# Performance work log

Hardware: AMD Instinct MI355X
Metric: run time of the kernel (lower is better)

Reference implementation:

```python
import jax, jax.numpy as jnp
import numpy as np

BETA = 0.25


def setup_inputs() -> dict:
    key = jax.random.key(0)
    k1, k2 = jax.random.split(key)
    B, T, D, K = 16, 4096, 256, 4096
    z_e = jax.random.normal(k1, (B, T, D), dtype=jnp.float32)
    # emulate uniform(-1/K, 1/K) init but any values work for correctness
    codebook = jax.random.uniform(k2, (K, D), dtype=jnp.float32,
                                  minval=-1.0 / K, maxval=1.0 / K)
    return {"z_e": z_e, "codebook": codebook}


def reference(z_e, codebook):
    D = codebook.shape[1]
    z_flat = z_e.reshape(-1, D)                                  # [N, D]
    # squared L2 distances: ||z||^2 + ||e||^2 - 2 z.e
    z_norm = jnp.sum(z_flat ** 2, axis=1, keepdims=True)          # [N, 1]
    e_norm = jnp.sum(codebook ** 2, axis=1)                       # [K]
    dist = z_norm + e_norm - 2.0 * jnp.matmul(z_flat, codebook.T) # [N, K]
    idx_flat = jnp.argmin(dist, axis=1)                           # [N]
    idx = idx_flat.reshape(z_e.shape[:-1])                        # [B, T]
    z_q = codebook[idx]                                           # [B, T, D]
    # commitment loss: beta * mse(stop_grad(z_q), z_e)
    loss = BETA * jnp.mean((jax.lax.stop_gradient(z_q) - z_e) ** 2)
    # straight-through estimator
    z_q_st = z_e + jax.lax.stop_gradient(z_q - z_e)
    return z_q_st, idx, loss
```

## Files before the change

kernel.cpp:

```cpp
#include <hip/hip_runtime.h>
#include <cfloat>

#define NROWS 65536
#define DIM   256
#define KCB   4096

#define EPS_WIN  1.8e-4f
#define CAND_CAP 16

typedef __attribute__((ext_vector_type(8))) short short8;
typedef __attribute__((ext_vector_type(4))) float f32x4;

__device__ inline unsigned short f2bf(float x) {
  unsigned int u = __float_as_uint(x);
  return (unsigned short)((u + 0x7fffu + ((u >> 16) & 1u)) >> 16);
}

__global__ void prep_norms_kernel(const float* __restrict__ z, const float* __restrict__ cb,
                                  unsigned short* __restrict__ zh, unsigned short* __restrict__ eh,
                                  float* __restrict__ znorm, float* __restrict__ enorm) {
  const int r    = blockIdx.x * 4 + (threadIdx.x >> 6);
  const int lane = threadIdx.x & 63;
  const float* src; unsigned short* dst; float* nrm; int row;
  if (r < NROWS) { src = z;  dst = zh; nrm = znorm; row = r; }
  else           { src = cb; dst = eh; nrm = enorm; row = r - NROWS; }
  const float4 v = ((const float4*)(src + (size_t)row * DIM))[lane];
  union { unsigned short us[4]; uint2 u2; } o;
  o.us[0] = f2bf(v.x); o.us[1] = f2bf(v.y); o.us[2] = f2bf(v.z); o.us[3] = f2bf(v.w);
  *(uint2*)(dst + (size_t)row * DIM + lane * 4) = o.u2;
  float s = v.x * v.x + v.y * v.y + v.z * v.z + v.w * v.w;
  #pragma unroll
  for (int off = 32; off > 0; off >>= 1) s += __shfl_down(s, off);
  if (lane == 0) nrm[row] = s;
}

__launch_bounds__(256, 2)
__global__ void screen_kernel(const unsigned short* __restrict__ zh,
                              const unsigned short* __restrict__ eh,
                              const float* __restrict__ znorm,
                              const float* __restrict__ enorm,
                              unsigned int* __restrict__ counts,
                              unsigned short* __restrict__ cands) {
  __shared__ __align__(16) unsigned short a_s[128 * 256];
  __shared__ __align__(16) unsigned short b_s[128 * 32];
  __shared__ float zn_s[128];
  __shared__ float tilemin_s[2][128];
  __shared__ unsigned int cnt_s[128];
  __shared__ unsigned short cand_s[128 * CAND_CAP];

  const int tid = threadIdx.x;
  const int wv  = tid >> 6;
  const int ln  = tid & 63;
  const int l15 = ln & 15;
  const int lg  = ln >> 4;
  const int wr  = wv >> 1;
  const int wc  = wv & 1;
  const int rbase = blockIdx.x * 128;

  if (tid < 128) { zn_s[tid] = znorm[rbase + tid]; cnt_s[tid] = 0u; }

  #pragma unroll 1
  for (int i = 0; i < 16; ++i) {
    const int gid = i * 256 + tid;
    const int row = gid >> 5, slot = gid & 31;
    const int sw  = slot ^ (row & 7);
    *(uint4*)(&a_s[row * 256 + sw * 8]) =
        *(const uint4*)(&zh[(size_t)(rbase + row) * 256 + slot * 8]);
  }
  __syncthreads();

  float znv[16];
  #pragma unroll
  for (int fr = 0; fr < 4; ++fr)
    #pragma unroll
    for (int q = 0; q < 4; ++q)
      znv[fr * 4 + q] = zn_s[wr * 64 + fr * 16 + lg * 4 + q];

  float rm[16];
  #pragma unroll
  for (int s = 0; s < 16; ++s) rm[s] = FLT_MAX;

  #pragma unroll 1
  for (int kt = 0; kt < KCB / 128; ++kt) {
    const int kcb0 = kt * 128;
    f32x4 acc[4][4];
    #pragma unroll
    for (int fr = 0; fr < 4; ++fr)
      #pragma unroll
      for (int fc = 0; fc < 4; ++fc)
        acc[fr][fc] = (f32x4){0.f, 0.f, 0.f, 0.f};

    #pragma unroll 1
    for (int dc = 0; dc < 8; ++dc) {
      __syncthreads();
      #pragma unroll
      for (int i = 0; i < 2; ++i) {
        const int c  = i * 64 + wv * 16 + l15;
        const int sw = lg ^ ((c >> 1) & 3);
        *(uint4*)(&b_s[c * 32 + sw * 8]) =
            *(const uint4*)(&eh[(size_t)(kcb0 + c) * 256 + dc * 32 + lg * 8]);
      }
      __syncthreads();

      short8 af[4];
      #pragma unroll
      for (int fr = 0; fr < 4; ++fr) {
        const int r = wr * 64 + fr * 16 + l15;
        const int sl = (dc * 4 + lg) ^ (r & 7);
        af[fr] = *(const short8*)(&a_s[r * 256 + sl * 8]);
      }
      short8 bf[4];
      #pragma unroll
      for (int fc = 0; fc < 4; ++fc) {
        const int c = wc * 64 + fc * 16 + l15;
        const int sw = lg ^ ((c >> 1) & 3);
        bf[fc] = *(const short8*)(&b_s[c * 32 + sw * 8]);
      }
      #pragma unroll
      for (int fr = 0; fr < 4; ++fr)
        #pragma unroll
        for (int fc = 0; fc < 4; ++fc)
          acc[fr][fc] = __builtin_amdgcn_mfma_f32_16x16x32_bf16(
              af[fr], bf[fc], acc[fr][fc], 0, 0, 0);
    }

    float en_[4];
    #pragma unroll
    for (int fc = 0; fc < 4; ++fc) en_[fc] = enorm[kcb0 + wc * 64 + fc * 16 + l15];

    float tm[16];
    #pragma unroll
    for (int s = 0; s < 16; ++s) tm[s] = FLT_MAX;

    #pragma unroll
    for (int fr = 0; fr < 4; ++fr)
      #pragma unroll
      for (int fc = 0; fc < 4; ++fc)
        #pragma unroll
        for (int q = 0; q < 4; ++q) {
          const float d_ = fmaf(-2.0f, acc[fr][fc][q], znv[fr * 4 + q] + en_[fc]);
          tm[fr * 4 + q] = fminf(tm[fr * 4 + q], d_);
        }

    float hv[16];
    #pragma unroll
    for (int s = 0; s < 16; ++s) {
      float v = tm[s];
      v = fminf(v, __shfl_xor(v, 1));
      v = fminf(v, __shfl_xor(v, 2));
      v = fminf(v, __shfl_xor(v, 4));
      v = fminf(v, __shfl_xor(v, 8));
      hv[s] = v;
      if (l15 == 0) {
        const int fr = s >> 2, q = s & 3;
        tilemin_s[wc][wr * 64 + fr * 16 + lg * 4 + q] = v;
      }
    }
    __syncthreads();

    float th[16];
    float guard = 1.0f;
    #pragma unroll
    for (int s = 0; s < 16; ++s) {
      const int fr = s >> 2, q = s & 3;
      const float other = tilemin_s[wc ^ 1][wr * 64 + fr * 16 + lg * 4 + q];
      const float m = fminf(rm[s], fminf(hv[s], other));
      rm[s] = m;
      th[s] = m + EPS_WIN;
      guard = fminf(guard, tm[s] - th[s]);
    }

    if (__any(guard <= 0.0f)) {
      #pragma unroll
      for (int fr = 0; fr < 4; ++fr)
        #pragma unroll
        for (int fc = 0; fc < 4; ++fc)
          #pragma unroll
          for (int q = 0; q < 4; ++q) {
            const float d_ = fmaf(-2.0f, acc[fr][fc][q], znv[fr * 4 + q] + en_[fc]);
            if (d_ <= th[fr * 4 + q]) {
              const int rl = wr * 64 + fr * 16 + lg * 4 + q;
              const unsigned int pos = atomicAdd(&cnt_s[rl], 1u);
              if (pos < CAND_CAP)
                cand_s[rl * CAND_CAP + pos] =
                    (unsigned short)(kcb0 + wc * 64 + fc * 16 + l15);
            }
          }
    }
  }

  __syncthreads();
  if (tid < 128) counts[rbase + tid] = cnt_s[tid];
  for (int i = tid; i < 128 * CAND_CAP; i += 256)
    cands[(size_t)rbase * CAND_CAP + i] = cand_s[i];
}

__global__ void rescore_kernel(const float* __restrict__ z, const float* __restrict__ cb,
                               const float* __restrict__ znorm, const float* __restrict__ enorm,
                               const unsigned int* __restrict__ counts,
                               const unsigned short* __restrict__ cands,
                               int* __restrict__ idx) {
  const int gw  = (blockIdx.x * 256 + threadIdx.x) >> 6;
  const int ln  = threadIdx.x & 63;
  const int row = gw * 4 + (ln >> 4);
  const int ci  = ln & 15;
  const unsigned int cnt = counts[row];

  float bv = FLT_MAX; int bk = 0x7fffffff;
  if (cnt <= CAND_CAP) {
    const int active = ci < (int)cnt;
    const int k = active ? (int)cands[(size_t)row * CAND_CAP + ci] : 0;
    const float4* zr = (const float4*)(z  + (size_t)row * DIM);
    const float4* er = (const float4*)(cb + (size_t)k   * DIM);
    float ax = 0.f, ay = 0.f, az = 0.f, aw = 0.f;
    #pragma unroll 4
    for (int d = 0; d < DIM / 4; ++d) {
      const float4 zv = zr[d], ev = er[d];
      ax = fmaf(zv.x, ev.x, ax); ay = fmaf(zv.y, ev.y, ay);
      az = fmaf(zv.z, ev.z, az); aw = fmaf(zv.w, ev.w, aw);
    }
    const float acc = (ax + ay) + (az + aw);
    const float dist = fmaf(-2.0f, acc, znorm[row] + enorm[k]);
    if (active) { bv = dist; bk = k; }
  }
  #pragma unroll
  for (int off = 1; off < 16; off <<= 1) {
    const float ov = __shfl_xor(bv, off);
    const int   ok = __shfl_xor(bk, off);
    if (ov < bv || (ov == bv && ok < bk)) { bv = ov; bk = ok; }
  }
  if (ci == 0 && cnt <= CAND_CAP) idx[row] = bk;
}

__global__ void fallback_kernel(const float* __restrict__ z, const float* __restrict__ cb,
                                const float* __restrict__ znorm, const float* __restrict__ enorm,
                                const unsigned int* __restrict__ counts,
                                int* __restrict__ idx) {
  __shared__ float bd_s[256];
  __shared__ int   bk_s[256];
  const int tid = threadIdx.x;
  for (int row = blockIdx.x; row < NROWS; row += gridDim.x) {
    if (counts[row] <= CAND_CAP) continue;
    const float zn = znorm[row];
    const float* zr = z + (size_t)row * DIM;
    float bv = FLT_MAX; int bk = 0x7fffffff;
    for (int k = tid; k < KCB; k += 256) {
      const float* er = cb + (size_t)k * DIM;
      float acc = 0.0f;
      #pragma unroll 8
      for (int d = 0; d < DIM; ++d) acc = fmaf(zr[d], er[d], acc);
      const float dist = fmaf(-2.0f, acc, zn + enorm[k]);
      if (dist < bv || (dist == bv && k < bk)) { bv = dist; bk = k; }
    }
    bd_s[tid] = bv; bk_s[tid] = bk;
    __syncthreads();
    for (int s = 128; s > 0; s >>= 1) {
      if (tid < s) {
        const float ov = bd_s[tid + s]; const int ok = bk_s[tid + s];
        if (ov < bd_s[tid] || (ov == bd_s[tid] && ok < bk_s[tid])) {
          bd_s[tid] = ov; bk_s[tid] = ok;
        }
      }
      __syncthreads();
    }
    if (tid == 0) idx[row] = bk_s[0];
    __syncthreads();
  }
}

__global__ void norms_kernel(const float* __restrict__ x, float* __restrict__ out) {
  const int row  = blockIdx.x * 4 + (threadIdx.x >> 6);
  const int lane = threadIdx.x & 63;
  const float4 v = ((const float4*)(x + (size_t)row * DIM))[lane];
  float s = v.x * v.x + v.y * v.y + v.z * v.z + v.w * v.w;
  #pragma unroll
  for (int off = 32; off > 0; off >>= 1) s += __shfl_down(s, off);
  if (lane == 0) out[row] = s;
}

#define BM 128
#define BK 128
#define BD 32
#define LSTR 36
__launch_bounds__(256, 2)
__global__ void argmin_kernel(const float* __restrict__ z,
                              const float* __restrict__ cb,
                              const float* __restrict__ znorm,
                              const float* __restrict__ enorm,
                              int* __restrict__ idx_out) {
  __shared__ float z_s[BM * LSTR];
  __shared__ float e_s[BK * LSTR];
  __shared__ float zn_s[BM];
  const int tid = threadIdx.x;
  const int tx = tid & 15;
  const int ty = tid >> 4;
  const int rbase = blockIdx.x * BM;
  if (tid < BM) zn_s[tid] = znorm[rbase + tid];
  float bestv[8]; int besti[8];
  #pragma unroll
  for (int i = 0; i < 8; ++i) { bestv[i] = FLT_MAX; besti[i] = 0; }
  for (int kc = 0; kc < KCB; kc += BK) {
    float acc[8][8];
    #pragma unroll
    for (int i = 0; i < 8; ++i)
      #pragma unroll
      for (int j = 0; j < 8; ++j) acc[i][j] = 0.0f;
    for (int dc = 0; dc < DIM; dc += BD) {
      __syncthreads();
      #pragma unroll
      for (int p = 0; p < 4; ++p) {
        const int el = p * 256 + tid;
        const int r  = el >> 3;
        const int c4 = (el & 7) * 4;
        *(float4*)(&z_s[r * LSTR + c4]) =
            *(const float4*)(z + (size_t)(rbase + r) * DIM + dc + c4);
        *(float4*)(&e_s[r * LSTR + c4]) =
            *(const float4*)(cb + (size_t)(kc + r) * DIM + dc + c4);
      }
      __syncthreads();
      #pragma unroll 1
      for (int dd = 0; dd < BD; dd += 4) {
        float4 b[8];
        #pragma unroll
        for (int j = 0; j < 8; ++j)
          b[j] = *(const float4*)(&e_s[(tx + 16 * j) * LSTR + dd]);
        #pragma unroll
        for (int i = 0; i < 8; ++i) {
          const float4 a = *(const float4*)(&z_s[(ty + 16 * i) * LSTR + dd]);
          #pragma unroll
          for (int j = 0; j < 8; ++j)
            acc[i][j] += a.x * b[j].x + a.y * b[j].y + a.z * b[j].z + a.w * b[j].w;
        }
      }
    }
    float en[8];
    #pragma unroll
    for (int j = 0; j < 8; ++j) en[j] = enorm[kc + tx + 16 * j];
    #pragma unroll
    for (int i = 0; i < 8; ++i) {
      const float zn = zn_s[ty + 16 * i];
      #pragma unroll
      for (int j = 0; j < 8; ++j) {
        const float t1 = zn + en[j];
        const float dist = t1 - 2.0f * acc[i][j];
        const int k = kc + tx + 16 * j;
        if (dist < bestv[i]) { bestv[i] = dist; besti[i] = k; }
      }
    }
  }
  #pragma unroll
  for (int i = 0; i < 8; ++i) {
    float lv = bestv[i]; int li = besti[i];
    #pragma unroll
    for (int off = 1; off < 16; off <<= 1) {
      const float ov = __shfl_xor(lv, off);
      const int   oi = __shfl_xor(li, off);
      if (ov < lv || (ov == lv && oi < li)) { lv = ov; li = oi; }
    }
    if (tx == 0) idx_out[rbase + ty + 16 * i] = li;
  }
}

__global__ void gather_kernel(const float* __restrict__ z,
                              const float* __restrict__ cb,
                              const int* __restrict__ idx,
                              float* __restrict__ out_zq,
                              float* __restrict__ out_idx,
                              float* __restrict__ partials) {
  const int row  = blockIdx.x * 4 + (threadIdx.x >> 6);
  const int lane = threadIdx.x & 63;
  const int k = idx[row];
  const float4 zv = ((const float4*)(z  + (size_t)row * DIM))[lane];
  const float4 ev = ((const float4*)(cb + (size_t)k   * DIM))[lane];
  float4 d, st;
  d.x = ev.x - zv.x; d.y = ev.y - zv.y; d.z = ev.z - zv.z; d.w = ev.w - zv.w;
  st.x = zv.x + d.x; st.y = zv.y + d.y; st.z = zv.z + d.z; st.w = zv.w + d.w;
  ((float4*)(out_zq + (size_t)row * DIM))[lane] = st;
  if (lane == 0) out_idx[row] = (float)k;
  float s = d.x * d.x + d.y * d.y + d.z * d.z + d.w * d.w;
  #pragma unroll
  for (int off = 32; off > 0; off >>= 1) s += __shfl_down(s, off);
  __shared__ float ps[4];
  if (lane == 0) ps[threadIdx.x >> 6] = s;
  __syncthreads();
  if (threadIdx.x == 0)
    partials[blockIdx.x] = (ps[0] + ps[1]) + (ps[2] + ps[3]);
}

__global__ void loss_kernel(const float* __restrict__ partials,
                            float* __restrict__ out_loss) {
  float s = 0.0f;
  for (int i = threadIdx.x; i < NROWS / 4; i += 256) s += partials[i];
  #pragma unroll
  for (int off = 32; off > 0; off >>= 1) s += __shfl_down(s, off);
  __shared__ float ps[4];
  if ((threadIdx.x & 63) == 0) ps[threadIdx.x >> 6] = s;
  __syncthreads();
  if (threadIdx.x == 0)
    *out_loss = 0.25f * (((ps[0] + ps[1]) + (ps[2] + ps[3])) *
                         (1.0f / (float)((size_t)NROWS * DIM)));
}

extern "C" void kernel_launch(void* const* d_in, const int* in_sizes, int n_in,
                              void* d_out, int out_size, void* d_ws, size_t ws_size,
                              hipStream_t stream) {
  const float* z  = (const float*)d_in[0];
  const float* cb = (const float*)d_in[1];

  float* out_zq   = (float*)d_out;
  float* out_idx  = out_zq + (size_t)NROWS * DIM;
  float* out_loss = out_idx + NROWS;

  char* w = (char*)d_ws;
  unsigned short* zh    = (unsigned short*)(w);
  unsigned short* eh    = (unsigned short*)(w + 33554432);
  float* enorm          = (float*)(w + 35651584);
  float* znorm          = (float*)(w + 35667968);
  int*   idx            = (int*)(w + 35930112);
  unsigned int* counts  = (unsigned int*)(w + 36192256);
  unsigned short* cands = (unsigned short*)(w + 36454400);
  float* partials       = (float*)(w + 38551552);
  const size_t NEED = 38617088;

  if (ws_size >= NEED) {
    hipLaunchKernelGGL(prep_norms_kernel, dim3((NROWS + KCB) / 4), dim3(256), 0, stream,
                       z, cb, zh, eh, znorm, enorm);
    hipLaunchKernelGGL(screen_kernel, dim3(NROWS / 128), dim3(256), 0, stream,
                       zh, eh, znorm, enorm, counts, cands);
    hipLaunchKernelGGL(rescore_kernel, dim3(NROWS / 16), dim3(256), 0, stream,
                       z, cb, znorm, enorm, counts, cands, idx);
    hipLaunchKernelGGL(fallback_kernel, dim3(256), dim3(256), 0, stream,
                       z, cb, znorm, enorm, counts, idx);
    hipLaunchKernelGGL(gather_kernel, dim3(NROWS / 4), dim3(256), 0, stream,
                       z, cb, idx, out_zq, out_idx, partials);
    hipLaunchKernelGGL(loss_kernel, dim3(1), dim3(256), 0, stream, partials, out_loss);
  } else {
    float* ws        = (float*)d_ws;
    float* enorm_l   = ws;
    float* znorm_l   = ws + KCB;
    int*   idx_l     = (int*)(ws + KCB + NROWS);
    float* partials_l= ws + KCB + 2 * NROWS;
    hipLaunchKernelGGL(norms_kernel, dim3(KCB / 4), dim3(256), 0, stream, cb, enorm_l);
    hipLaunchKernelGGL(norms_kernel, dim3(NROWS / 4), dim3(256), 0, stream, z, znorm_l);
    hipLaunchKernelGGL(argmin_kernel, dim3(NROWS / BM), dim3(256), 0, stream,
                       z, cb, znorm_l, enorm_l, idx_l);
    hipLaunchKernelGGL(gather_kernel, dim3(NROWS / 4), dim3(256), 0, stream,
                       z, cb, idx_l, out_zq, out_idx, partials_l);
    hipLaunchKernelGGL(loss_kernel, dim3(1), dim3(256), 0, stream, partials_l, out_loss);
  }
}
```

Measured before the change: 520.5 us.

## Register-prefetch next codebook chunk and re-layout A tile into per-chunk panels

Codebook bf16 chunks are now loaded into registers one iteration ahead, so the global load for the next dc chunk overlaps with the MFMA work on the current one instead of stalling between the two barriers. The A tile in shared memory is reorganized into 8 panels of 128x32 with a swizzle matching the B tile, and the thread-to-element mapping for B loads is changed to contiguous 16-byte segments. This adds register pressure and one extra redundant prefetch at the final iteration, which wraps around to chunk 0.

```diff
diff --git a/kernel.cpp b/kernel.cpp
--- a/kernel.cpp
+++ b/kernel.cpp
@@ -41,7 +41,7 @@
                               const float* __restrict__ enorm,
                               unsigned int* __restrict__ counts,
                               unsigned short* __restrict__ cands) {
-  __shared__ __align__(16) unsigned short a_s[128 * 256];
+  __shared__ __align__(16) unsigned short a_s[8][128][32];
   __shared__ __align__(16) unsigned short b_s[128 * 32];
   __shared__ float zn_s[128];
   __shared__ float tilemin_s[2][128];
@@ -63,11 +63,24 @@
   for (int i = 0; i < 16; ++i) {
     const int gid = i * 256 + tid;
     const int row = gid >> 5, slot = gid & 31;
-    const int sw  = slot ^ (row & 7);
-    *(uint4*)(&a_s[row * 256 + sw * 8]) =
+    const int ch = slot >> 2, s4 = slot & 3;
+    const int sw = s4 ^ ((row >> 1) & 3);
+    *(uint4*)(&a_s[ch][row][sw * 8]) =
         *(const uint4*)(&zh[(size_t)(rbase + row) * 256 + slot * 8]);
   }
-  __syncthreads();
+
+  int pc[2], ps[2];
+  #pragma unroll
+  for (int t = 0; t < 2; ++t) {
+    const int o = wv * 2048 + t * 1024 + ln * 16;
+    pc[t] = o >> 6;
+    ps[t] = (o >> 4) & 3;
+  }
+
+  uint4 pre[2];
+  #pragma unroll
+  for (int t = 0; t < 2; ++t)
+    pre[t] = *(const uint4*)(&eh[(size_t)pc[t] * 256 + ps[t] * 8]);
 
   float znv[16];
   #pragma unroll
@@ -79,6 +92,8 @@
   float rm[16];
   #pragma unroll
   for (int s = 0; s < 16; ++s) rm[s] = FLT_MAX;
+
+  __syncthreads();
 
   #pragma unroll 1
   for (int kt = 0; kt < KCB / 128; ++kt) {
@@ -94,20 +109,26 @@
     for (int dc = 0; dc < 8; ++dc) {
       __syncthreads();
       #pragma unroll
-      for (int i = 0; i < 2; ++i) {
-        const int c  = i * 64 + wv * 16 + l15;
-        const int sw = lg ^ ((c >> 1) & 3);
-        *(uint4*)(&b_s[c * 32 + sw * 8]) =
-            *(const uint4*)(&eh[(size_t)(kcb0 + c) * 256 + dc * 32 + lg * 8]);
+      for (int t = 0; t < 2; ++t) {
+        const int sw = ps[t] ^ ((pc[t] >> 1) & 3);
+        *(uint4*)(&b_s[pc[t] * 32 + sw * 8]) = pre[t];
       }
       __syncthreads();
+      {
+        const int ndc = (dc + 1) & 7;
+        const int nkt = (dc == 7) ? ((kt + 1) & (KCB / 128 - 1)) : kt;
+        const size_t nb = (size_t)(nkt * 128) * 256 + ndc * 32;
+        #pragma unroll
+        for (int t = 0; t < 2; ++t)
+          pre[t] = *(const uint4*)(&eh[nb + (size_t)pc[t] * 256 + ps[t] * 8]);
+      }
 
       short8 af[4];
       #pragma unroll
       for (int fr = 0; fr < 4; ++fr) {
         const int r = wr * 64 + fr * 16 + l15;
-        const int sl = (dc * 4 + lg) ^ (r & 7);
-        af[fr] = *(const short8*)(&a_s[r * 256 + sl * 8]);
+        const int sl = lg ^ ((r >> 1) & 3);
+        af[fr] = *(const short8*)(&a_s[dc][r][sl * 8]);
       }
       short8 bf[4];
       #pragma unroll
```

Measured after the change: 653.7 us. +25.6%, slower.
